# Optimization experiments

Hardware: AMD Instinct MI355X
Metric: run time of the kernel (lower is better)

## Reference

```python
import jax, jax.numpy as jnp
import numpy as np

N_NODES = 50000


def gcn_conv(x, W, b, src, dst, num_nodes):
    # x: [N, Fin] -> lin -> [N, Fout]; gather source feats per edge, scatter-add at dst.
    h = x @ W                                   # [N, Fout]
    msg = h[src]                                # [E, Fout]  (message = x_j, no edge_weight)
    out = jax.ops.segment_sum(msg, dst, num_segments=num_nodes)  # [N, Fout]
    return out + b


def setup_inputs() -> dict:
    key = jax.random.key(0)
    k1, k2, k3, k4 = jax.random.split(key, 4)
    x = jax.random.normal(k1, (N_NODES, 128), dtype=jnp.float32)
    edge_index = jax.random.randint(k2, (2, 800000), 0, N_NODES, dtype=jnp.int64)
    W1 = jax.random.normal(k3, (128, 256), dtype=jnp.float32) * (1.0 / np.sqrt(128))
    b1 = jnp.zeros((256,), dtype=jnp.float32)
    W2 = jax.random.normal(k4, (256, 40), dtype=jnp.float32) * (1.0 / np.sqrt(256))
    b2 = jnp.zeros((40,), dtype=jnp.float32)
    return {"x": x, "edge_index": edge_index, "W1": W1, "b1": b1, "W2": W2, "b2": b2}


def reference(x, edge_index, W1, b1, W2, b2):
    src, dst = edge_index[0], edge_index[1]
    h = gcn_conv(x, W1, b1, src, dst, N_NODES)
    h = jax.nn.relu(h)
    out = gcn_conv(h, W2, b2, src, dst, N_NODES)
    return out
```

## Files before the change

kernel.cpp:

```cpp
#include <hip/hip_runtime.h>

typedef unsigned int u32;
typedef unsigned short u16;
using f32x4 = __attribute__((ext_vector_type(4))) float;
using f32x2 = __attribute__((ext_vector_type(2))) float;
using i32x4 = __attribute__((ext_vector_type(4))) int;
using s16x8 = __attribute__((ext_vector_type(8))) short;
using s16x4 = __attribute__((ext_vector_type(4))) short;

__device__ __forceinline__ u16 rne_bf16(float f) {
  u32 u = __float_as_uint(f);
  u += 0x7FFF + ((u >> 16) & 1);
  return (u16)(u >> 16);
}
__device__ __forceinline__ float bf_lo(u32 u) { return __uint_as_float(u << 16); }
__device__ __forceinline__ float bf_hi(u32 u) { return __uint_as_float(u & 0xFFFF0000u); }

#define NBX 12500
#define CAP 64

__global__ __launch_bounds__(256) void setup_k(const float* __restrict__ x, u32* __restrict__ xb,
                                               int n2, int4* __restrict__ cnt4, int nc4,
                                               const float* __restrict__ W1, u16* __restrict__ W1t,
                                               const float* __restrict__ W2, u16* __restrict__ W2t) {
  int b = blockIdx.x, t = threadIdx.x;
  if (b < NBX) {
    int i = b * 256 + t;
    if (i < nc4) cnt4[i] = make_int4(0, 0, 0, 0);
    if (i < n2) {
      f32x2 v = __builtin_nontemporal_load((const f32x2*)x + i);
      xb[i] = (u32)rne_bf16(v.x) | ((u32)rne_bf16(v.y) << 16);
    }
  } else if (b < NBX + 128) {
    int idx = (b - NBX) * 256 + t;
    int n = idx >> 7, k = idx & 127;
    W1t[idx] = rne_bf16(W1[k * 256 + n]);
  } else {
    int idx = (b - NBX - 128) * 256 + t;
    int c = idx >> 8, k = idx & 255;
    W2t[idx] = (c < 40) ? rne_bf16(W2[k * 40 + c]) : (u16)0;
  }
}

__global__ __launch_bounds__(256) void scatterB_k(const int* __restrict__ srcv,
                                                  const int* __restrict__ dstv,
                                                  int* __restrict__ cnt,
                                                  int* __restrict__ adj,
                                                  int E, int nbin) {
  int p = blockIdx.x & 7;
  int lo = p * nbin, hi = lo + nbin;
  int g = blockIdx.x >> 3;
  int ngroups = gridDim.x >> 3;
  int stride4 = ngroups * blockDim.x * 4;
  for (int i0 = (g * blockDim.x + threadIdx.x) * 4; i0 < E; i0 += stride4) {
    if (i0 + 3 < E) {
      i32x4 d4 = __builtin_nontemporal_load((const i32x4*)(dstv + i0));
      #pragma unroll
      for (int j = 0; j < 4; ++j) {
        int d = d4[j];
        if (d >= lo && d < hi) {
          int s = __builtin_nontemporal_load(srcv + i0 + j);
          int pos = atomicAdd(&cnt[d], 1);
          if (pos < CAP) adj[(size_t)d * CAP + pos] = s;
        }
      }
    } else {
      for (int i = i0; i < E; ++i) {
        int d = dstv[i];
        if (d >= lo && d < hi) {
          int pos = atomicAdd(&cnt[d], 1);
          if (pos < CAP) adj[(size_t)d * CAP + pos] = srcv[i];
        }
      }
    }
  }
}

__global__ void agg128_k(const u32* __restrict__ xb, const int* __restrict__ adj,
                         const int* __restrict__ cnt, u32* __restrict__ aggb, int n) {
  int lane = threadIdx.x & 63;
  int node = blockIdx.x * 4 + (threadIdx.x >> 6);
  if (node >= n) return;
  int deg = cnt[node]; if (deg > CAP) deg = CAP;
  const int* ab = adj + (size_t)node * CAP;
  float ax = 0.f, ay = 0.f;
  int i = 0;
  for (; i + 8 <= deg; i += 8) {
    u32 u0 = xb[(size_t)ab[i] * 64 + lane];
    u32 u1 = xb[(size_t)ab[i + 1] * 64 + lane];
    u32 u2 = xb[(size_t)ab[i + 2] * 64 + lane];
    u32 u3 = xb[(size_t)ab[i + 3] * 64 + lane];
    u32 u4 = xb[(size_t)ab[i + 4] * 64 + lane];
    u32 u5 = xb[(size_t)ab[i + 5] * 64 + lane];
    u32 u6 = xb[(size_t)ab[i + 6] * 64 + lane];
    u32 u7 = xb[(size_t)ab[i + 7] * 64 + lane];
    ax += ((bf_lo(u0) + bf_lo(u1)) + (bf_lo(u2) + bf_lo(u3)))
        + ((bf_lo(u4) + bf_lo(u5)) + (bf_lo(u6) + bf_lo(u7)));
    ay += ((bf_hi(u0) + bf_hi(u1)) + (bf_hi(u2) + bf_hi(u3)))
        + ((bf_hi(u4) + bf_hi(u5)) + (bf_hi(u6) + bf_hi(u7)));
  }
  for (; i + 2 <= deg; i += 2) {
    u32 u0 = xb[(size_t)ab[i] * 64 + lane];
    u32 u1 = xb[(size_t)ab[i + 1] * 64 + lane];
    ax += bf_lo(u0) + bf_lo(u1); ay += bf_hi(u0) + bf_hi(u1);
  }
  for (; i < deg; ++i) {
    u32 u = xb[(size_t)ab[i] * 64 + lane];
    ax += bf_lo(u); ay += bf_hi(u);
  }
  aggb[(size_t)node * 64 + lane] = (u32)rne_bf16(ax) | ((u32)rne_bf16(ay) << 16);
}

__global__ __launch_bounds__(64) void fused_k(const u16* __restrict__ Ab,
                                              const u16* __restrict__ W1t,
                                              const float* __restrict__ b1,
                                              const u16* __restrict__ W2t,
                                              u32* __restrict__ zb, int M) {
  __shared__ short slab[2][16 * 34];
  const int l = threadIdx.x;
  const int p = l & 15, g = l >> 4;
  const int m0 = blockIdx.x * 32;

  s16x8 af[2][4];
  #pragma unroll
  for (int rt = 0; rt < 2; ++rt) {
    int mrow = m0 + rt * 16 + p;
    int mload = (mrow < M) ? mrow : (M - 1);
    const u16* arow = Ab + (size_t)mload * 128 + g * 8;
    #pragma unroll
    for (int kt = 0; kt < 4; ++kt) af[rt][kt] = *(const s16x8*)(arow + kt * 32);
  }

  f32x4 acc2[2][3];
  #pragma unroll
  for (int rt = 0; rt < 2; ++rt)
    #pragma unroll
    for (int n2 = 0; n2 < 3; ++n2) acc2[rt][n2] = (f32x4){0.f, 0.f, 0.f, 0.f};

  #pragma unroll 2
  for (int s = 0; s < 8; ++s) {
    const int n0 = 2 * s, n1 = 2 * s + 1;
    const u16* w0 = W1t + (size_t)(n0 * 16 + p) * 128 + g * 8;
    const u16* w1 = W1t + (size_t)(n1 * 16 + p) * 128 + g * 8;
    s16x8 wA[4], wB[4];
    #pragma unroll
    for (int kt = 0; kt < 4; ++kt) {
      wA[kt] = *(const s16x8*)(w0 + kt * 32);
      wB[kt] = *(const s16x8*)(w1 + kt * 32);
    }
    float4 bva = *(const float4*)(b1 + n0 * 16 + g * 4);
    float4 bvb = *(const float4*)(b1 + n1 * 16 + g * 4);
    #pragma unroll
    for (int rt = 0; rt < 2; ++rt) {
      f32x4 aA = {0.f, 0.f, 0.f, 0.f};
      f32x4 aB = {0.f, 0.f, 0.f, 0.f};
      #pragma unroll
      for (int kt = 0; kt < 4; ++kt) {
        aA = __builtin_amdgcn_mfma_f32_16x16x32_bf16(wA[kt], af[rt][kt], aA, 0, 0, 0);
        aB = __builtin_amdgcn_mfma_f32_16x16x32_bf16(wB[kt], af[rt][kt], aB, 0, 0, 0);
      }
      s16x4 pa, pb;
      pa[0] = (short)rne_bf16(fmaxf(aA[0] + bva.x, 0.f));
      pa[1] = (short)rne_bf16(fmaxf(aA[1] + bva.y, 0.f));
      pa[2] = (short)rne_bf16(fmaxf(aA[2] + bva.z, 0.f));
      pa[3] = (short)rne_bf16(fmaxf(aA[3] + bva.w, 0.f));
      pb[0] = (short)rne_bf16(fmaxf(aB[0] + bvb.x, 0.f));
      pb[1] = (short)rne_bf16(fmaxf(aB[1] + bvb.y, 0.f));
      pb[2] = (short)rne_bf16(fmaxf(aB[2] + bvb.z, 0.f));
      pb[3] = (short)rne_bf16(fmaxf(aB[3] + bvb.w, 0.f));
      *(s16x4*)&slab[rt][p * 34 + g * 4] = pa;
      *(s16x4*)&slab[rt][p * 34 + 16 + g * 4] = pb;
    }
    #pragma unroll
    for (int n2 = 0; n2 < 3; ++n2) {
      s16x8 wf = *(const s16x8*)(W2t + (size_t)(n2 * 16 + p) * 256 + s * 32 + g * 8);
      #pragma unroll
      for (int rt = 0; rt < 2; ++rt) {
        s16x8 a2 = *(const s16x8*)&slab[rt][p * 34 + g * 8];
        acc2[rt][n2] = __builtin_amdgcn_mfma_f32_16x16x32_bf16(wf, a2, acc2[rt][n2], 0, 0, 0);
      }
    }
  }

  #pragma unroll
  for (int rt = 0; rt < 2; ++rt) {
    int mrow = m0 + rt * 16 + p;
    if (mrow < M) {
      #pragma unroll
      for (int n2 = 0; n2 < 3; ++n2) {
        int c0 = n2 * 16 + g * 4;
        if (c0 < 40) {
          uint2 o;
          o.x = (u32)rne_bf16(acc2[rt][n2][0]) | ((u32)rne_bf16(acc2[rt][n2][1]) << 16);
          o.y = (u32)rne_bf16(acc2[rt][n2][2]) | ((u32)rne_bf16(acc2[rt][n2][3]) << 16);
          *(uint2*)(zb + (size_t)mrow * 20 + n2 * 8 + g * 2) = o;
        }
      }
    }
  }
}

__global__ void agg40_k(const u32* __restrict__ zb, const int* __restrict__ adj,
                        const int* __restrict__ cnt, const float* __restrict__ bias,
                        float* __restrict__ outp, int n) {
  int hl = threadIdx.x & 31;
  int node = blockIdx.x * 8 + (threadIdx.x >> 5);
  if (node >= n || hl >= 20) return;
  int deg = cnt[node]; if (deg > CAP) deg = CAP;
  const int* ab = adj + (size_t)node * CAP;
  float ax = 0.f, ay = 0.f;
  int i = 0;
  for (; i + 4 <= deg; i += 4) {
    u32 u0 = zb[(size_t)ab[i] * 20 + hl];
    u32 u1 = zb[(size_t)ab[i + 1] * 20 + hl];
    u32 u2 = zb[(size_t)ab[i + 2] * 20 + hl];
    u32 u3 = zb[(size_t)ab[i + 3] * 20 + hl];
    ax += (bf_lo(u0) + bf_lo(u1)) + (bf_lo(u2) + bf_lo(u3));
    ay += (bf_hi(u0) + bf_hi(u1)) + (bf_hi(u2) + bf_hi(u3));
  }
  for (; i < deg; ++i) {
    u32 u = zb[(size_t)ab[i] * 20 + hl];
    ax += bf_lo(u); ay += bf_hi(u);
  }
  float2 bv = ((const float2*)bias)[hl];
  ((float2*)(outp + (size_t)node * 40))[hl] = make_float2(ax + bv.x, ay + bv.y);
}

extern "C" void kernel_launch(void* const* d_in, const int* in_sizes, int n_in,
                              void* d_out, int out_size, void* d_ws, size_t ws_size,
                              hipStream_t stream) {
  const float* x  = (const float*)d_in[0];
  const int*   ei = (const int*)d_in[1];
  const float* W1 = (const float*)d_in[2];
  const float* b1 = (const float*)d_in[3];
  const float* W2 = (const float*)d_in[4];
  const float* b2 = (const float*)d_in[5];
  float* out = (float*)d_out;

  int N = in_sizes[0] / 128;
  int E = in_sizes[1] / 2;
  const int* src = ei;
  const int* dst = ei + E;

  char* ws = (char*)d_ws;
  size_t off = 0;
  auto carve = [&](size_t bytes) {
    char* p = ws + off;
    off += (bytes + 255) & ~(size_t)255;
    return p;
  };
  u32* xb    = (u32*)carve((size_t)N * 128 * 2);
  u32* aggb  = (u32*)carve((size_t)N * 128 * 2);
  u16* W1t   = (u16*)carve(256 * 128 * 2);
  u16* W2t   = (u16*)carve(48 * 256 * 2);
  u32* zbuf  = (u32*)carve((size_t)N * 20 * 4);
  int* cnt   = (int*)carve((size_t)N * 4);
  int* adj   = (int*)carve((size_t)N * CAP * 4);

  int nbin = (N + 7) / 8;
  int nc4 = (N + 3) / 4;

  setup_k<<<NBX + 128 + 48, 256, 0, stream>>>(x, xb, N * 64,
                                              (int4*)cnt, nc4, W1, W1t, W2, W2t);
  scatterB_k<<<1024, 256, 0, stream>>>(src, dst, cnt, adj, E, nbin);
  agg128_k<<<(N + 3) / 4, 256, 0, stream>>>(xb, adj, cnt, aggb, N);
  fused_k<<<(N + 31) / 32, 64, 0, stream>>>((const u16*)aggb, W1t, b1, W2t, zbuf, N);
  agg40_k<<<(N + 7) / 8, 256, 0, stream>>>(zbuf, adj, cnt, b2, out, N);
}
```

Before: 136.3 us.

## Merge edge scatter with bf16 conversion into one kernel, split out counter zeroing

Measured after the change: 129.3 us. -5.1%, faster.

```diff
diff --git a/kernel.cpp b/kernel.cpp
--- a/kernel.cpp
+++ b/kernel.cpp
@@ -18,61 +18,64 @@
 
 #define NBX 12500
 #define CAP 64
-
-__global__ __launch_bounds__(256) void setup_k(const float* __restrict__ x, u32* __restrict__ xb,
-                                               int n2, int4* __restrict__ cnt4, int nc4,
-                                               const float* __restrict__ W1, u16* __restrict__ W1t,
-                                               const float* __restrict__ W2, u16* __restrict__ W2t) {
+#define SCAT 2048
+
+__global__ void zero_k(int4* __restrict__ cnt4, int nc4) {
+  int i = blockIdx.x * 256 + threadIdx.x;
+  if (i < nc4) cnt4[i] = make_int4(0, 0, 0, 0);
+}
+
+__global__ __launch_bounds__(256) void mega_k(const int* __restrict__ srcv,
+                                              const int* __restrict__ dstv,
+                                              int* __restrict__ cnt,
+                                              int* __restrict__ adj,
+                                              int E, int nbin,
+                                              const float* __restrict__ x, u32* __restrict__ xb,
+                                              int n2,
+                                              const float* __restrict__ W1, u16* __restrict__ W1t,
+                                              const float* __restrict__ W2, u16* __restrict__ W2t) {
   int b = blockIdx.x, t = threadIdx.x;
-  if (b < NBX) {
-    int i = b * 256 + t;
-    if (i < nc4) cnt4[i] = make_int4(0, 0, 0, 0);
+  if (b < SCAT) {
+    int p = b & 7;
+    int lo = p * nbin, hi = lo + nbin;
+    int g = b >> 3;
+    int ngroups = SCAT >> 3;
+    int stride4 = ngroups * 256 * 4;
+    for (int i0 = (g * 256 + t) * 4; i0 < E; i0 += stride4) {
+      if (i0 + 3 < E) {
+        i32x4 d4 = *(const i32x4*)(dstv + i0);
+        #pragma unroll
+        for (int j = 0; j < 4; ++j) {
+          int d = d4[j];
+          if (d >= lo && d < hi) {
+            int pos = atomicAdd(&cnt[d], 1);
+            if (pos < CAP) adj[(size_t)d * CAP + pos] = srcv[i0 + j];
+          }
+        }
+      } else {
+        for (int i = i0; i < E; ++i) {
+          int d = dstv[i];
+          if (d >= lo && d < hi) {
+            int pos = atomicAdd(&cnt[d], 1);
+            if (pos < CAP) adj[(size_t)d * CAP + pos] = srcv[i];
+          }
+        }
+      }
+    }
+  } else if (b < SCAT + NBX) {
+    int i = (b - SCAT) * 256 + t;
     if (i < n2) {
-      f32x2 v = __builtin_nontemporal_load((const f32x2*)x + i);
+      f32x2 v = *((const f32x2*)x + i);
       xb[i] = (u32)rne_bf16(v.x) | ((u32)rne_bf16(v.y) << 16);
     }
-  } else if (b < NBX + 128) {
-    int idx = (b - NBX) * 256 + t;
+  } else if (b < SCAT + NBX + 128) {
+    int idx = (b - SCAT - NBX) * 256 + t;
     int n = idx >> 7, k = idx & 127;
     W1t[idx] = rne_bf16(W1[k * 256 + n]);
   } else {
-    int idx = (b - NBX - 128) * 256 + t;
+    int idx = (b - SCAT - NBX - 128) * 256 + t;
     int c = idx >> 8, k = idx & 255;
     W2t[idx] = (c < 40) ? rne_bf16(W2[k * 40 + c]) : (u16)0;
-  }
-}
-
-__global__ __launch_bounds__(256) void scatterB_k(const int* __restrict__ srcv,
-                                                  const int* __restrict__ dstv,
-                                                  int* __restrict__ cnt,
-                                                  int* __restrict__ adj,
-                                                  int E, int nbin) {
-  int p = blockIdx.x & 7;
-  int lo = p * nbin, hi = lo + nbin;
-  int g = blockIdx.x >> 3;
-  int ngroups = gridDim.x >> 3;
-  int stride4 = ngroups * blockDim.x * 4;
-  for (int i0 = (g * blockDim.x + threadIdx.x) * 4; i0 < E; i0 += stride4) {
-    if (i0 + 3 < E) {
-      i32x4 d4 = __builtin_nontemporal_load((const i32x4*)(dstv + i0));
-      #pragma unroll
-      for (int j = 0; j < 4; ++j) {
-        int d = d4[j];
-        if (d >= lo && d < hi) {
-          int s = __builtin_nontemporal_load(srcv + i0 + j);
-          int pos = atomicAdd(&cnt[d], 1);
-          if (pos < CAP) adj[(size_t)d * CAP + pos] = s;
-        }
-      }
-    } else {
-      for (int i = i0; i < E; ++i) {
-        int d = dstv[i];
-        if (d >= lo && d < hi) {
-          int pos = atomicAdd(&cnt[d], 1);
-          if (pos < CAP) adj[(size_t)d * CAP + pos] = srcv[i];
-        }
-      }
-    }
   }
 }
 
@@ -260,9 +263,9 @@
   int nbin = (N + 7) / 8;
   int nc4 = (N + 3) / 4;
 
-  setup_k<<<NBX + 128 + 48, 256, 0, stream>>>(x, xb, N * 64,
-                                              (int4*)cnt, nc4, W1, W1t, W2, W2t);
-  scatterB_k<<<1024, 256, 0, stream>>>(src, dst, cnt, adj, E, nbin);
+  zero_k<<<(nc4 + 255) / 256, 256, 0, stream>>>((int4*)cnt, nc4);
+  mega_k<<<SCAT + NBX + 128 + 48, 256, 0, stream>>>(src, dst, cnt, adj, E, nbin,
+                                                    x, xb, N * 64, W1, W1t, W2, W2t);
   agg128_k<<<(N + 3) / 4, 256, 0, stream>>>(xb, adj, cnt, aggb, N);
   fused_k<<<(N + 31) / 32, 64, 0, stream>>>((const u16*)aggb, W1t, b1, W2t, zbuf, N);
   agg40_k<<<(N + 7) / 8, 256, 0, stream>>>(zbuf, adj, cnt, b2, out, N);
```
